# Kernel optimization log

Hardware: AMD Instinct MI355X
Metric: run time of the kernel (lower is better)

Reference implementation:

```python
import jax, jax.numpy as jnp
import numpy as np

SHIFT = 1  # self.shift_direction fixed to +1 (random +/-1 at init in original)


def setup_inputs() -> dict:
    key = jax.random.key(0)
    k1, k2 = jax.random.split(key)
    x = jax.random.normal(k1, (1024, 28, 64, 28), dtype=jnp.float32)
    W = jax.random.normal(k2, (128, 3, 32, 3), dtype=jnp.float32)
    return {"x": x, "W": W}


def reference(x, W):
    # einsum 'lkij -> likj': (1024,28,64,28) -> (1024,64,28,28)
    t = jnp.einsum('lkij->likj', x)
    # view as (N=1024, C=1, H=28, W=1792)
    t = t.reshape(1024, 1, 28, 1792)
    # unfold kernel (3,1), padding (1,0): patches along H -> (1024, 3, 28, 1792)
    tp = jnp.pad(t, ((0, 0), (0, 0), (1, 1), (0, 0)))
    t = jnp.stack([tp[:, 0, kh:kh + 28, :] for kh in range(3)], axis=1)
    # (1024,3,28,1792) == (1024,3,28,64,28) == (1024,3,56,32,28) contiguously
    t = t.reshape(1024, 3, 56, 32, 28)
    # cyclic shift along merged dim of size 56
    t = jnp.roll(t, SHIFT, axis=2)
    # split 56 -> (28,2) and sum over the 2
    t = t.reshape(1024, 3, 28, 2, 32, 28).sum(axis=3)  # (1024,3,28,32,28)
    # second unfold: view as (1024, 2688, 28, 1), kernel (3,1), pad (1,0)
    # equivalent: pad last dim (the H=28) and stack 3 shifted slices after channel dims
    tp = jnp.pad(t, ((0, 0), (0, 0), (0, 0), (0, 0), (1, 1)))
    t3 = jnp.stack([tp[..., kh:kh + 28] for kh in range(3)], axis=4)  # (1024,3,28,32,3,28)
    # final contraction with weights (128,3,32,3)
    return jnp.einsum('mlnjko,iljk->mino', t3, W)  # (1024,128,28,28)
```

## Files before the change

### kernel.cpp

```cpp
#include <hip/hip_runtime.h>


typedef _Float16 f16x8 __attribute__((ext_vector_type(8)));
typedef float    f32x4 __attribute__((ext_vector_type(4)));

#define PG  4
#define PVN 36
#define RP  104

__global__ void w_prep_kernel(const float* __restrict__ W, _Float16* __restrict__ Ah) {
    int id = blockIdx.x * 256 + threadIdx.x;
    if (id >= 3 * 128 * 96) return;
    int r  = id % 96;
    int t  = id / 96;
    int co = t & 127;
    int kw = t >> 7;
    Ah[id] = (_Float16)W[co * 288 + (r >> 5) * 96 + (r & 31) * 3 + kw];
}

__global__ __launch_bounds__(256, 3) void mfma_shiftconv_kernel(
        const float* __restrict__ x,
        const _Float16* __restrict__ Ah,
        float* __restrict__ out) {
    __shared__ _Float16 T6L[PG * PVN * RP];

    const int p0  = blockIdx.x * PG;
    const int l   = blockIdx.y;
    const int tid = threadIdx.x;
    const float* __restrict__ xl = x + (size_t)l * (28 * 64 * 28);

    {
        f32x4 z = {0.f, 0.f, 0.f, 0.f};
        f32x4* T4 = (f32x4*)T6L;
        for (int i = tid; i < (PG * PVN * RP) / 8; i += 256) T4[i] = z;
    }
    __syncthreads();

    for (int pr = tid; pr < PG * 96; pr += 256) {
        int p_loc = pr / 96;
        int r     = pr % 96;
        int kh    = r >> 5;
        int u     = r & 31;
        int p_abs = p0 + p_loc;
        int h1    = (p_abs + 27) % 28;

        const float* s0 = nullptr;
        const float* s1 = nullptr;
        int hh0 = p_abs + kh - 1;
        if (hh0 >= 0 && hh0 < 28) {
            int q = 8 * hh0 + u;
            s0 = xl + ((q % 28) * 64 + 2 * hh0 + (q / 28)) * 28;
        }
        int hh1 = h1 + kh - 1;
        if (hh1 >= 0 && hh1 < 28) {
            int q = 8 * hh1 + 4 + u;
            s1 = xl + ((q % 28) * 64 + 2 * hh1 + 1 + (q / 28)) * 28;
        }

        _Float16* dst = &T6L[(p_loc * PVN + 1) * RP + r];
        #pragma unroll
        for (int v = 0; v < 28; v += 4) {
            f32x4 a = {0.f, 0.f, 0.f, 0.f};
            f32x4 b = {0.f, 0.f, 0.f, 0.f};
            if (s0) a = *(const f32x4*)(s0 + v);
            if (s1) b = *(const f32x4*)(s1 + v);
            dst[(v + 0) * RP] = (_Float16)(a.x + b.x);
            dst[(v + 1) * RP] = (_Float16)(a.y + b.y);
            dst[(v + 2) * RP] = (_Float16)(a.z + b.z);
            dst[(v + 3) * RP] = (_Float16)(a.w + b.w);
        }
    }
    __syncthreads();

    const int lane = tid & 63;
    const int wid  = tid >> 6;
    const int wm   = wid >> 1;
    const int wn   = wid & 1;
    const int ln   = lane & 15;
    const int kb   = lane >> 4;

    f32x4 acc[4][4];
    {
        f32x4 zz = {0.f, 0.f, 0.f, 0.f};
        #pragma unroll
        for (int a2 = 0; a2 < 4; ++a2)
            #pragma unroll
            for (int b2 = 0; b2 < 4; ++b2) acc[a2][b2] = zz;
    }

    #pragma unroll
    for (int kw = 0; kw < 3; ++kw) {
        #pragma unroll
        for (int kf = 0; kf < 3; ++kf) {
            const int rr = 32 * kf + 8 * kb;
            f16x8 afr[4];
            #pragma unroll
            for (int mf = 0; mf < 4; ++mf) {
                int co = 64 * wm + 16 * mf + ln;
                afr[mf] = *(const f16x8*)(Ah + ((kw * 128 + co) * 96 + rr));
            }
            #pragma unroll
            for (int nfl = 0; nfl < 4; ++nfl) {
                int nf = 4 * wn + nfl;
                int pv = (nf & 1) * 16 + ln + kw;
                f16x8 bfr = *(const f16x8*)&T6L[((nf >> 1) * PVN + pv) * RP + rr];
                #pragma unroll
                for (int mf = 0; mf < 4; ++mf)
                    acc[mf][nfl] = __builtin_amdgcn_mfma_f32_16x16x32_f16(
                        afr[mf], bfr, acc[mf][nfl], 0, 0, 0);
            }
        }
    }

    #pragma unroll
    for (int nfl = 0; nfl < 4; ++nfl) {
        int nf = 4 * wn + nfl;
        int o  = (nf & 1) * 16 + ln;
        if (o < 28) {
            int p_abs = p0 + (nf >> 1);
            #pragma unroll
            for (int mf = 0; mf < 4; ++mf) {
                int co = 64 * wm + 16 * mf + 4 * kb;
                float* op = out + (((size_t)l * 128 + co) * 28 + p_abs) * 28 + o;
                #pragma unroll
                for (int q = 0; q < 4; ++q) op[(size_t)q * 784] = acc[mf][nfl][q];
            }
        }
    }
}

__global__ void fallback_shiftconv_kernel(
        const float* __restrict__ x,
        const float* __restrict__ W,
        float* __restrict__ out) {
    __shared__ float T6F[3 * 32 * 32];

    const int p = blockIdx.x;
    const int l = blockIdx.y;
    const int tid = threadIdx.x;

    const float* __restrict__ xl = x + (size_t)l * (28 * 64 * 28);
    const int h1 = (p + 27) % 28;

    for (int e = tid; e < 3072; e += 128) {
        int kh = e >> 10;
        int u  = (e >> 5) & 31;
        int pv = e & 31;
        int v  = pv - 1;
        float val = 0.f;
        if (v >= 0 && v < 28) {
            int hh0 = p + kh - 1;
            if (hh0 >= 0 && hh0 < 28) {
                int q  = 8 * hh0 + u;
                val += xl[((q % 28) * 64 + 2 * hh0 + (q / 28)) * 28 + v];
            }
            int hh1 = h1 + kh - 1;
            if (hh1 >= 0 && hh1 < 28) {
                int q  = 8 * hh1 + 4 + u;
                val += xl[((q % 28) * 64 + 2 * hh1 + 1 + (q / 28)) * 28 + v];
            }
        }
        T6F[e] = val;
    }
    __syncthreads();

    const int g  = tid & 31;
    const int hq = tid >> 5;
    const int ob = 7 * hq;

    float acc[4][7];
    #pragma unroll
    for (int m = 0; m < 4; ++m)
        #pragma unroll
        for (int d = 0; d < 7; ++d) acc[m][d] = 0.f;

    for (int kh = 0; kh < 3; ++kh) {
        for (int u = 0; u < 32; ++u) {
            const float* tl = &T6F[(kh * 32 + u) * 32 + ob];
            float tv[9];
            #pragma unroll
            for (int t2 = 0; t2 < 9; ++t2) tv[t2] = tl[t2];

            #pragma unroll
            for (int kw = 0; kw < 3; ++kw) {
                const int off = kh * 96 + u * 3 + kw;
                float w0 = W[(4 * g + 0) * 288 + off];
                float w1 = W[(4 * g + 1) * 288 + off];
                float w2 = W[(4 * g + 2) * 288 + off];
                float w3 = W[(4 * g + 3) * 288 + off];
                #pragma unroll
                for (int d = 0; d < 7; ++d) {
                    const float t = tv[d + kw];
                    acc[0][d] += w0 * t;
                    acc[1][d] += w1 * t;
                    acc[2][d] += w2 * t;
                    acc[3][d] += w3 * t;
                }
            }
        }
    }

    const size_t base = (((size_t)l * 128 + 4 * g) * 28 + p) * 28 + ob;
    #pragma unroll
    for (int m = 0; m < 4; ++m)
        #pragma unroll
        for (int d = 0; d < 7; ++d)
            out[base + (size_t)m * 784 + d] = acc[m][d];
}

extern "C" void kernel_launch(void* const* d_in, const int* in_sizes, int n_in,
                              void* d_out, int out_size, void* d_ws, size_t ws_size,
                              hipStream_t stream) {
    (void)in_sizes; (void)n_in; (void)out_size;
    const float* x = (const float*)d_in[0];
    const float* W = (const float*)d_in[1];
    float* out = (float*)d_out;

    if (ws_size >= 36864 * sizeof(_Float16)) {
        _Float16* Ah = (_Float16*)d_ws;
        w_prep_kernel<<<144, 256, 0, stream>>>(W, Ah);
        mfma_shiftconv_kernel<<<dim3(7, 1024), 256, 0, stream>>>(x, Ah, out);
    } else {
        fallback_shiftconv_kernel<<<dim3(28, 1024), 128, 0, stream>>>(x, W, out);
    }
}
```

Measured before the change: 666.8 us.

## Loop over batch items per block with double-buffered LDS and register prefetch

Each block now processes eight batch items in sequence. It prefetches the next item's input into registers while the current item's MFMA and output stores run, then writes it into a second LDS buffer. Gather addresses are computed once, and the padding rows are zeroed only once. This aims to hide global load latency and amortize setup. The cost is lower occupancy, more register pressure and a smaller grid.

```diff
diff --git a/kernel.cpp b/kernel.cpp
--- a/kernel.cpp
+++ b/kernel.cpp
@@ -5,8 +5,10 @@
 typedef float    f32x4 __attribute__((ext_vector_type(4)));
 
 #define PG  4
-#define PVN 36
+#define PVN 34
 #define RP  104
+#define NL  8
+#define TILE_HALVES (PG * PVN * RP)
 
 __global__ void w_prep_kernel(const float* __restrict__ W, _Float16* __restrict__ Ah) {
     int id = blockIdx.x * 256 + threadIdx.x;
@@ -18,59 +20,15 @@
     Ah[id] = (_Float16)W[co * 288 + (r >> 5) * 96 + (r & 31) * 3 + kw];
 }
 
-__global__ __launch_bounds__(256, 3) void mfma_shiftconv_kernel(
+__global__ __launch_bounds__(256, 2) void mfma_shiftconv_kernel(
         const float* __restrict__ x,
         const _Float16* __restrict__ Ah,
         float* __restrict__ out) {
-    __shared__ _Float16 T6L[PG * PVN * RP];
+    __shared__ __align__(16) _Float16 T6L[2][TILE_HALVES];
 
     const int p0  = blockIdx.x * PG;
-    const int l   = blockIdx.y;
+    const int l0  = blockIdx.y * NL;
     const int tid = threadIdx.x;
-    const float* __restrict__ xl = x + (size_t)l * (28 * 64 * 28);
-
-    {
-        f32x4 z = {0.f, 0.f, 0.f, 0.f};
-        f32x4* T4 = (f32x4*)T6L;
-        for (int i = tid; i < (PG * PVN * RP) / 8; i += 256) T4[i] = z;
-    }
-    __syncthreads();
-
-    for (int pr = tid; pr < PG * 96; pr += 256) {
-        int p_loc = pr / 96;
-        int r     = pr % 96;
-        int kh    = r >> 5;
-        int u     = r & 31;
-        int p_abs = p0 + p_loc;
-        int h1    = (p_abs + 27) % 28;
-
-        const float* s0 = nullptr;
-        const float* s1 = nullptr;
-        int hh0 = p_abs + kh - 1;
-        if (hh0 >= 0 && hh0 < 28) {
-            int q = 8 * hh0 + u;
-            s0 = xl + ((q % 28) * 64 + 2 * hh0 + (q / 28)) * 28;
-        }
-        int hh1 = h1 + kh - 1;
-        if (hh1 >= 0 && hh1 < 28) {
-            int q = 8 * hh1 + 4 + u;
-            s1 = xl + ((q % 28) * 64 + 2 * hh1 + 1 + (q / 28)) * 28;
-        }
-
-        _Float16* dst = &T6L[(p_loc * PVN + 1) * RP + r];
-        #pragma unroll
-        for (int v = 0; v < 28; v += 4) {
-            f32x4 a = {0.f, 0.f, 0.f, 0.f};
-            f32x4 b = {0.f, 0.f, 0.f, 0.f};
-            if (s0) a = *(const f32x4*)(s0 + v);
-            if (s1) b = *(const f32x4*)(s1 + v);
-            dst[(v + 0) * RP] = (_Float16)(a.x + b.x);
-            dst[(v + 1) * RP] = (_Float16)(a.y + b.y);
-            dst[(v + 2) * RP] = (_Float16)(a.z + b.z);
-            dst[(v + 3) * RP] = (_Float16)(a.w + b.w);
-        }
-    }
-    __syncthreads();
 
     const int lane = tid & 63;
     const int wid  = tid >> 6;
@@ -79,53 +37,154 @@
     const int ln   = lane & 15;
     const int kb   = lane >> 4;
 
-    f32x4 acc[4][4];
+    int  offs0[3], offs1[3], wraddr[3];
+    bool has0[3], has1[3];
+    #pragma unroll
+    for (int t3 = 0; t3 < 3; ++t3) {
+        int task  = tid + 256 * t3;
+        int row   = task >> 1;
+        int half  = task & 1;
+        int p_loc = row / 96;
+        int r     = row % 96;
+        int kh    = r >> 5;
+        int u     = r & 31;
+        int v0    = 14 * half;
+        int p_abs = p0 + p_loc;
+        int h1    = (p_abs + 27) % 28;
+
+        int hh0 = p_abs + kh - 1;
+        has0[t3] = (hh0 >= 0 && hh0 < 28);
+        offs0[t3] = 0;
+        if (has0[t3]) {
+            int q = 8 * hh0 + u;
+            offs0[t3] = ((q % 28) * 64 + 2 * hh0 + (q / 28)) * 28 + v0;
+        }
+        int hh1 = h1 + kh - 1;
+        has1[t3] = (hh1 >= 0 && hh1 < 28);
+        offs1[t3] = 0;
+        if (has1[t3]) {
+            int q = 8 * hh1 + 4 + u;
+            offs1[t3] = ((q % 28) * 64 + 2 * hh1 + 1 + (q / 28)) * 28 + v0;
+        }
+        wraddr[t3] = (p_loc * PVN + 1 + v0) * RP + r;
+    }
+
     {
-        f32x4 zz = {0.f, 0.f, 0.f, 0.f};
-        #pragma unroll
-        for (int a2 = 0; a2 < 4; ++a2)
-            #pragma unroll
-            for (int b2 = 0; b2 < 4; ++b2) acc[a2][b2] = zz;
-    }
-
-    #pragma unroll
-    for (int kw = 0; kw < 3; ++kw) {
-        #pragma unroll
-        for (int kf = 0; kf < 3; ++kf) {
-            const int rr = 32 * kf + 8 * kb;
-            f16x8 afr[4];
-            #pragma unroll
-            for (int mf = 0; mf < 4; ++mf) {
-                int co = 64 * wm + 16 * mf + ln;
-                afr[mf] = *(const f16x8*)(Ah + ((kw * 128 + co) * 96 + rr));
-            }
-            #pragma unroll
-            for (int nfl = 0; nfl < 4; ++nfl) {
-                int nf = 4 * wn + nfl;
-                int pv = (nf & 1) * 16 + ln + kw;
-                f16x8 bfr = *(const f16x8*)&T6L[((nf >> 1) * PVN + pv) * RP + rr];
-                #pragma unroll
-                for (int mf = 0; mf < 4; ++mf)
-                    acc[mf][nfl] = __builtin_amdgcn_mfma_f32_16x16x32_f16(
-                        afr[mf], bfr, acc[mf][nfl], 0, 0, 0);
-            }
-        }
-    }
-
-    #pragma unroll
-    for (int nfl = 0; nfl < 4; ++nfl) {
-        int nf = 4 * wn + nfl;
-        int o  = (nf & 1) * 16 + ln;
-        if (o < 28) {
-            int p_abs = p0 + (nf >> 1);
-            #pragma unroll
-            for (int mf = 0; mf < 4; ++mf) {
-                int co = 64 * wm + 16 * mf + 4 * kb;
-                float* op = out + (((size_t)l * 128 + co) * 28 + p_abs) * 28 + o;
-                #pragma unroll
-                for (int q = 0; q < 4; ++q) op[(size_t)q * 784] = acc[mf][nfl][q];
-            }
-        }
+        f32x4 z = {0.f, 0.f, 0.f, 0.f};
+        f32x4* T4 = (f32x4*)&T6L[0][0];
+        for (int i = tid; i < (2 * TILE_HALVES) / 8; i += 256) T4[i] = z;
+    }
+    __syncthreads();
+
+    const size_t XSTR = 28 * 64 * 28;
+    float2 sa[3][7], sb[3][7];
+
+    {
+        const float* xl = x + (size_t)l0 * XSTR;
+        #pragma unroll
+        for (int t3 = 0; t3 < 3; ++t3) {
+            #pragma unroll
+            for (int k = 0; k < 7; ++k) {
+                float2 a = {0.f, 0.f}, b = {0.f, 0.f};
+                if (has0[t3]) a = *(const float2*)(xl + offs0[t3] + 2 * k);
+                if (has1[t3]) b = *(const float2*)(xl + offs1[t3] + 2 * k);
+                sa[t3][k] = a; sb[t3][k] = b;
+            }
+        }
+        #pragma unroll
+        for (int t3 = 0; t3 < 3; ++t3) {
+            _Float16* w = &T6L[0][wraddr[t3]];
+            #pragma unroll
+            for (int k = 0; k < 7; ++k) {
+                w[(2 * k + 0) * RP] = (_Float16)(sa[t3][k].x + sb[t3][k].x);
+                w[(2 * k + 1) * RP] = (_Float16)(sa[t3][k].y + sb[t3][k].y);
+            }
+        }
+    }
+    __syncthreads();
+
+    int cur = 0;
+    for (int t = 0; t < NL; ++t) {
+        const int  l    = l0 + t;
+        const bool more = (t + 1 < NL);
+
+        if (more) {
+            const float* xl = x + (size_t)(l + 1) * XSTR;
+            #pragma unroll
+            for (int t3 = 0; t3 < 3; ++t3) {
+                #pragma unroll
+                for (int k = 0; k < 7; ++k) {
+                    float2 a = {0.f, 0.f}, b = {0.f, 0.f};
+                    if (has0[t3]) a = *(const float2*)(xl + offs0[t3] + 2 * k);
+                    if (has1[t3]) b = *(const float2*)(xl + offs1[t3] + 2 * k);
+                    sa[t3][k] = a; sb[t3][k] = b;
+                }
+            }
+        }
+
+        f32x4 acc[4][4];
+        {
+            f32x4 zz = {0.f, 0.f, 0.f, 0.f};
+            #pragma unroll
+            for (int a2 = 0; a2 < 4; ++a2)
+                #pragma unroll
+                for (int b2 = 0; b2 < 4; ++b2) acc[a2][b2] = zz;
+        }
+        const _Float16* Tc = &T6L[cur][0];
+        #pragma unroll
+        for (int kw = 0; kw < 3; ++kw) {
+            #pragma unroll
+            for (int kf = 0; kf < 3; ++kf) {
+                const int rr = 32 * kf + 8 * kb;
+                f16x8 afr[4];
+                #pragma unroll
+                for (int mf = 0; mf < 4; ++mf) {
+                    int co = 64 * wm + 16 * mf + ln;
+                    afr[mf] = *(const f16x8*)(Ah + ((kw * 128 + co) * 96 + rr));
+                }
+                #pragma unroll
+                for (int nfl = 0; nfl < 4; ++nfl) {
+                    int nf = 4 * wn + nfl;
+                    int pv = (nf & 1) * 16 + ln + kw;
+                    f16x8 bfr = *(const f16x8*)&Tc[((nf >> 1) * PVN + pv) * RP + rr];
+                    #pragma unroll
+                    for (int mf = 0; mf < 4; ++mf)
+                        acc[mf][nfl] = __builtin_amdgcn_mfma_f32_16x16x32_f16(
+                            afr[mf], bfr, acc[mf][nfl], 0, 0, 0);
+                }
+            }
+        }
+
+        #pragma unroll
+        for (int nfl = 0; nfl < 4; ++nfl) {
+            int nf = 4 * wn + nfl;
+            int o  = (nf & 1) * 16 + ln;
+            if (o < 28) {
+                int p_abs = p0 + (nf >> 1);
+                #pragma unroll
+                for (int mf = 0; mf < 4; ++mf) {
+                    int co = 64 * wm + 16 * mf + 4 * kb;
+                    float* op = out + (((size_t)l * 128 + co) * 28 + p_abs) * 28 + o;
+                    #pragma unroll
+                    for (int q = 0; q < 4; ++q) op[(size_t)q * 784] = acc[mf][nfl][q];
+                }
+            }
+        }
+
+        if (more) {
+            _Float16* Tn = &T6L[cur ^ 1][0];
+            #pragma unroll
+            for (int t3 = 0; t3 < 3; ++t3) {
+                _Float16* w = &Tn[wraddr[t3]];
+                #pragma unroll
+                for (int k = 0; k < 7; ++k) {
+                    w[(2 * k + 0) * RP] = (_Float16)(sa[t3][k].x + sb[t3][k].x);
+                    w[(2 * k + 1) * RP] = (_Float16)(sa[t3][k].y + sb[t3][k].y);
+                }
+            }
+            __syncthreads();
+        }
+        cur ^= 1;
     }
 }
 
@@ -219,7 +278,7 @@
     if (ws_size >= 36864 * sizeof(_Float16)) {
         _Float16* Ah = (_Float16*)d_ws;
         w_prep_kernel<<<144, 256, 0, stream>>>(W, Ah);
-        mfma_shiftconv_kernel<<<dim3(7, 1024), 256, 0, stream>>>(x, Ah, out);
+        mfma_shiftconv_kernel<<<dim3(7, 128), 256, 0, stream>>>(x, Ah, out);
     } else {
         fallback_shiftconv_kernel<<<dim3(28, 1024), 128, 0, stream>>>(x, W, out);
     }
```

New measurement: 1.007 ms. +51.0%, slower.
